# Kernel optimization log

Measured on AMD Instinct MI355X. Metric: run time of the kernel, lower is better.

The kernel has to match this reference:

```python
import jax, jax.numpy as jnp
import numpy as np

K_CONV = 4
NUM_HEADS = 16
NUM_KV_HEADS = 8
D_HEAD = 128
ROPE_THETA = 10000.0
EPS = 1e-6
NEG_INF = -1e30


def canon_b(x, w):
    """Canon-B: causal depthwise conv1d (kernel K_CONV) with residual.
    x: [B, S, C], w: [C, K_CONV]. out[t] = x[t] + sum_k w[:,k] * x[t-k]."""
    S = x.shape[1]
    xp = jnp.pad(x, ((0, 0), (K_CONV - 1, 0), (0, 0)))
    conv = sum(xp[:, K_CONV - 1 - k:K_CONV - 1 - k + S, :] * w[:, k] for k in range(K_CONV))
    return x + conv


def rms_norm(x, w):
    var = jnp.mean(x * x, axis=-1, keepdims=True)
    return x * jax.lax.rsqrt(var + EPS) * w


def rope_cos_sin(S, d):
    inv_freq = 1.0 / (ROPE_THETA ** (jnp.arange(0, d, 2, dtype=jnp.float32) / d))
    freqs = jnp.arange(S, dtype=jnp.float32)[:, None] * inv_freq  # [S, d/2]
    emb = jnp.concatenate([freqs, freqs], axis=-1)  # [S, d]
    return jnp.cos(emb), jnp.sin(emb)


def rotate_half(x):
    x1, x2 = jnp.split(x, 2, axis=-1)
    return jnp.concatenate([-x2, x1], axis=-1)


def setup_inputs() -> dict:
    key = jax.random.key(0)
    ks = jax.random.split(key, 8)
    B, S, D = 2, 2048, 2048
    Dkv = NUM_KV_HEADS * D_HEAD
    s = 0.02
    return {
        "hidden_states": jax.random.normal(ks[0], (B, S, D), jnp.float32),
        "Wq": jax.random.normal(ks[1], (D, D), jnp.float32) * s,
        "Wk": jax.random.normal(ks[2], (Dkv, D), jnp.float32) * s,
        "Wv": jax.random.normal(ks[3], (Dkv, D), jnp.float32) * s,
        "Wo": jax.random.normal(ks[4], (D, D), jnp.float32) * s,
        "canon_q_w": jax.random.normal(ks[5], (D, K_CONV), jnp.float32) * 0.1,
        "canon_k_w": jax.random.normal(ks[6], (Dkv, K_CONV), jnp.float32) * 0.1,
        "canon_v_w": jax.random.normal(ks[7], (Dkv, K_CONV), jnp.float32) * 0.1,
        "q_norm_w": jnp.ones((D_HEAD,), jnp.float32),
        "k_norm_w": jnp.ones((D_HEAD,), jnp.float32),
    }


def reference(hidden_states, Wq, Wk, Wv, Wo, canon_q_w, canon_k_w, canon_v_w, q_norm_w, k_norm_w):
    B, S, D = hidden_states.shape
    scale = 1.0 / np.sqrt(D_HEAD)
    groups = NUM_HEADS // NUM_KV_HEADS

    # QKV projections (no bias)
    q = hidden_states @ Wq.T
    k = hidden_states @ Wk.T
    v = hidden_states @ Wv.T

    # Canon-B causal depthwise conv on flat projections
    q = canon_b(q, canon_q_w)
    k = canon_b(k, canon_k_w)
    v = canon_b(v, canon_v_w)

    # Split heads: [B, S, H, d_head]
    q = q.reshape(B, S, NUM_HEADS, D_HEAD)
    k = k.reshape(B, S, NUM_KV_HEADS, D_HEAD)
    v = v.reshape(B, S, NUM_KV_HEADS, D_HEAD)

    # qk RMSNorm over d_head
    q = rms_norm(q, q_norm_w)
    k = rms_norm(k, k_norm_w)

    # RoPE
    cos, sin = rope_cos_sin(S, D_HEAD)  # [S, d_head]
    cos = cos[None, :, None, :]
    sin = sin[None, :, None, :]
    q = q * cos + rotate_half(q) * sin
    k = k * cos + rotate_half(k) * sin

    # [B, H, S, d_head]
    q = q.transpose(0, 2, 1, 3)
    k = k.transpose(0, 2, 1, 3)
    v = v.transpose(0, 2, 1, 3)

    # GQA: repeat kv heads
    k = jnp.repeat(k, groups, axis=1)
    v = jnp.repeat(v, groups, axis=1)

    # Causal attention (eager)
    scores = jnp.einsum("bhqd,bhkd->bhqk", q, k) * scale
    causal = jnp.tril(jnp.ones((S, S), bool))
    scores = jnp.where(causal, scores, NEG_INF)
    probs = jax.nn.softmax(scores, axis=-1)
    attn = jnp.einsum("bhqk,bhkd->bhqd", probs, v)

    out = attn.transpose(0, 2, 1, 3).reshape(B, S, D)
    return out @ Wo.T
```

## Files before the change

### kernel.cpp

```cpp
#include <hip/hip_runtime.h>
#include <hip/hip_bf16.h>

typedef __bf16 bf16;
typedef __bf16 bf16x8 __attribute__((ext_vector_type(8)));
typedef float  floatx4 __attribute__((ext_vector_type(4)));

#define AS1 __attribute__((address_space(1)))
#define AS3 __attribute__((address_space(3)))

#define B_    2
#define S_    2048
#define D_    2048
#define H_    16
#define KVH_  8
#define DH_   128
#define M_    4096
#define NQKV_ 4096

__global__ __launch_bounds__(256) void prep_kernel(const float* __restrict__ hidden,
                                                   const float* __restrict__ Wq,
                                                   const float* __restrict__ Wk,
                                                   const float* __restrict__ Wv,
                                                   const float* __restrict__ Wo,
                                                   bf16* __restrict__ X,
                                                   bf16* __restrict__ Wcat,
                                                   bf16* __restrict__ Wob,
                                                   float* __restrict__ cost,
                                                   float* __restrict__ sint) {
    size_t u = (size_t)blockIdx.x * 256 + threadIdx.x;
    if (u < 5242880) {
        const float* src; bf16* dst; size_t off;
        if (u < 2097152)      { src = hidden; dst = X;              off = u; }
        else if (u < 3145728) { src = Wq;     dst = Wcat;           off = u - 2097152; }
        else if (u < 3670016) { src = Wk;     dst = Wcat + 4194304; off = u - 3145728; }
        else if (u < 4194304) { src = Wv;     dst = Wcat + 6291456; off = u - 3670016; }
        else                  { src = Wo;     dst = Wob;            off = u - 4194304; }
        float4 v = *(const float4*)(src + off * 4);
        union { bf16 h[4]; double d; } uu;
        uu.h[0] = (bf16)v.x; uu.h[1] = (bf16)v.y; uu.h[2] = (bf16)v.z; uu.h[3] = (bf16)v.w;
        *(double*)(dst + off * 4) = uu.d;
    } else {
        int r = (int)(u - 5242880);
        int t = r >> 6, fi = r & 63;
        float inv = expf(-9.210340371976184f * (float)fi * (1.0f / 64.0f));
        float ang = (float)t * inv;
        cost[r] = cosf(ang);
        sint[r] = sinf(ang);
    }
}

__global__ __launch_bounds__(512, 2) void gemm_bt8(const bf16* __restrict__ A,
                                                   const bf16* __restrict__ Bw,
                                                   bf16* __restrict__ C,
                                                   int M, int N, int K) {
    __shared__ __align__(16) bf16 Als[4][256 * 32];
    __shared__ __align__(16) bf16 Bls[4][256 * 32];
    int tid  = threadIdx.x;
    int wave = tid >> 6, lane = tid & 63;
    int quad = lane >> 4, l16 = lane & 15;
    int wr = wave >> 2, wc = wave & 3;

    int nbx = N >> 8;
    int wg  = (blockIdx.x & 7) * ((int)gridDim.x >> 3) + (blockIdx.x >> 3);
    int by  = wg / nbx, bx = wg % nbx;
    long bm0 = (long)by << 8, bn0 = (long)bx << 8;

    int slot8 = ((quad ^ ((l16 ^ (l16 >> 2)) & 3)) << 3);

    int srow   = tid >> 2;
    int schunk = (tid & 3) ^ ((srow ^ (srow >> 2)) & 3);
    const bf16* Asrc = A  + (bm0 + srow) * K + schunk * 8;
    const bf16* Bsrc = Bw + (bn0 + srow) * K + schunk * 8;
    size_t ldoff = (size_t)128 * K;

    floatx4 acc[8][4] = {};
    int NT = K >> 5;

#define STAGE_A8(t) { int d_ = (t) & 3; long k0_ = (long)(t) << 5;                                   \
    __builtin_amdgcn_global_load_lds((AS1 const unsigned int*)(Asrc + k0_),                          \
                                     (AS3 unsigned int*)(&Als[d_][0] + tid * 8), 16, 0, 0);          \
    __builtin_amdgcn_global_load_lds((AS1 const unsigned int*)(Asrc + ldoff + k0_),                  \
                                     (AS3 unsigned int*)(&Als[d_][0] + tid * 8 + 4096), 16, 0, 0); }
#define STAGE_B8(t) { int d_ = (t) & 3; long k0_ = (long)(t) << 5;                                   \
    __builtin_amdgcn_global_load_lds((AS1 const unsigned int*)(Bsrc + k0_),                          \
                                     (AS3 unsigned int*)(&Bls[d_][0] + tid * 8), 16, 0, 0);          \
    __builtin_amdgcn_global_load_lds((AS1 const unsigned int*)(Bsrc + ldoff + k0_),                  \
                                     (AS3 unsigned int*)(&Bls[d_][0] + tid * 8 + 4096), 16, 0, 0); }

    STAGE_A8(0); STAGE_B8(0);
    STAGE_A8(1); STAGE_B8(1);
    STAGE_A8(2); STAGE_B8(2);
    asm volatile("s_waitcnt vmcnt(8)" ::: "memory");
    __builtin_amdgcn_s_barrier();

    for (int u = 0; u < NT; ++u) {
        const bf16* Ab = &Als[u & 3][0];
        const bf16* Bb = &Bls[u & 3][0];
        bf16x8 af[8], bfr[4];
        #pragma unroll
        for (int mt = 0; mt < 8; ++mt) {
            int row = wr * 128 + mt * 16 + l16;
            af[mt] = *(const bf16x8*)(Ab + row * 32 + slot8);
        }
        #pragma unroll
        for (int nt = 0; nt < 4; ++nt) {
            int col = wc * 64 + nt * 16 + l16;
            bfr[nt] = *(const bf16x8*)(Bb + col * 32 + slot8);
        }
        if (u + 3 < NT) { STAGE_A8(u + 3); STAGE_B8(u + 3); }
        #pragma unroll
        for (int mt = 0; mt < 8; ++mt)
            #pragma unroll
            for (int nt = 0; nt < 4; ++nt)
                acc[mt][nt] = __builtin_amdgcn_mfma_f32_16x16x32_bf16(af[mt], bfr[nt], acc[mt][nt], 0, 0, 0);
        if (u < NT - 3)       { asm volatile("s_waitcnt vmcnt(8)" ::: "memory"); }
        else if (u == NT - 3) { asm volatile("s_waitcnt vmcnt(4)" ::: "memory"); }
        else                  { asm volatile("s_waitcnt vmcnt(0)" ::: "memory"); }
        __builtin_amdgcn_s_barrier();
    }
#undef STAGE_A8
#undef STAGE_B8
    #pragma unroll
    for (int mt = 0; mt < 8; ++mt) {
        #pragma unroll
        for (int nt = 0; nt < 4; ++nt) {
            long row = bm0 + wr * 128 + mt * 16 + quad * 4;
            long col = bn0 + wc * 64 + nt * 16 + l16;
            #pragma unroll
            for (int r = 0; r < 4; ++r)
                C[(row + r) * N + col] = (bf16)acc[mt][nt][r];
        }
    }
}

#define BM 128
#define BN 128
#define BK 64
template <typename CT>
__global__ __launch_bounds__(256) void gemm_bt(const bf16* __restrict__ A,
                                               const bf16* __restrict__ Bw,
                                               CT* __restrict__ C,
                                               int M, int N, int K) {
    __shared__ __align__(16) bf16 Als[BM * BK];
    __shared__ __align__(16) bf16 Bls[BN * BK];
    int tid  = threadIdx.x;
    int wave = tid >> 6, lane = tid & 63;
    int quad = lane >> 4, l16 = lane & 15;
    int wm = (wave >> 1) << 6;
    int wn = (wave & 1) << 6;

    long bm0 = (long)blockIdx.y * BM;
    long bn0 = (long)blockIdx.x * BN;
    const bf16* Ab = A  + bm0 * K;
    const bf16* Bb = Bw + bn0 * K;

    int srow = wave * 32 + (lane >> 3);
    int scol = ((lane & 7) ^ (lane >> 3)) << 3;
    int sdst = (wave * 32 + (lane >> 3)) * BK + ((lane & 7) << 3);

    floatx4 acc[4][4] = {};

    for (int k0 = 0; k0 < K; k0 += BK) {
        #pragma unroll
        for (int i = 0; i < 4; ++i) {
            const bf16* ga = Ab + (long)(srow + i * 8) * K + k0 + scol;
            const bf16* gb = Bb + (long)(srow + i * 8) * K + k0 + scol;
            __builtin_amdgcn_global_load_lds((AS1 const unsigned int*)ga,
                                             (AS3 unsigned int*)(Als + sdst + i * 512), 16, 0, 0);
            __builtin_amdgcn_global_load_lds((AS1 const unsigned int*)gb,
                                             (AS3 unsigned int*)(Bls + sdst + i * 512), 16, 0, 0);
        }
        __syncthreads();
        #pragma unroll
        for (int ks = 0; ks < 2; ++ks) {
            bf16x8 af[4], bfr[4];
            #pragma unroll
            for (int t = 0; t < 4; ++t) {
                int row = wm + t * 16 + l16;
                int g = (ks * 4 + quad) ^ (row & 7);
                af[t] = *(const bf16x8*)(Als + row * BK + (g << 3));
            }
            #pragma unroll
            for (int t = 0; t < 4; ++t) {
                int row = wn + t * 16 + l16;
                int g = (ks * 4 + quad) ^ (row & 7);
                bfr[t] = *(const bf16x8*)(Bls + row * BK + (g << 3));
            }
            #pragma unroll
            for (int mt = 0; mt < 4; ++mt)
                #pragma unroll
                for (int nt = 0; nt < 4; ++nt)
                    acc[mt][nt] = __builtin_amdgcn_mfma_f32_16x16x32_bf16(af[mt], bfr[nt], acc[mt][nt], 0, 0, 0);
        }
        __syncthreads();
    }
    #pragma unroll
    for (int mt = 0; mt < 4; ++mt) {
        #pragma unroll
        for (int nt = 0; nt < 4; ++nt) {
            long row = bm0 + wm + mt * 16 + quad * 4;
            long col = bn0 + wn + nt * 16 + l16;
            #pragma unroll
            for (int r = 0; r < 4; ++r)
                C[(row + r) * N + col] = (CT)acc[mt][nt][r];
        }
    }
}

__global__ __launch_bounds__(256, 4) void canon_kernel(const bf16* __restrict__ QKV,
                                                       const float* __restrict__ wq,
                                                       const float* __restrict__ wk,
                                                       const float* __restrict__ wv,
                                                       const float* __restrict__ qnw,
                                                       const float* __restrict__ knw,
                                                       const float* __restrict__ cost,
                                                       const float* __restrict__ sint,
                                                       bf16* __restrict__ qf,
                                                       bf16* __restrict__ kf,
                                                       bf16* __restrict__ vfrag) {
    __shared__ __align__(16) bf16 vtile[32 * 520];
    int tid  = threadIdx.x;
    int wid  = blockIdx.x * 4 + (tid >> 6);
    int lane = tid & 63;
    int b  = wid >> 11;
    int g  = (wid >> 8) & 7;
    int c  = wid & 255;
    int t0 = c << 3;
    int ch = (g << 9) + (lane << 3);

    const float* wrow; int cw;
    if (g < 4)      { wrow = wq; cw = ch; }
    else if (g < 6) { wrow = wk; cw = ch - 2048; }
    else            { wrow = wv; cw = ch - 3072; }

    float4 w4[8];
    #pragma unroll
    for (int j = 0; j < 8; ++j) w4[j] = *(const float4*)(wrow + (cw + j) * 4);

    union U8 { float4 v; bf16 h[8]; };
    const bf16* srcb = QKV + (size_t)((b << 11) + t0) * 4096 + ch;

    float xm1[8], xm2[8], xm3[8];
    if (t0 > 0) {
        U8 u1, u2, u3;
        u1.v = *(const float4*)(srcb - 4096);
        u2.v = *(const float4*)(srcb - 2 * 4096);
        u3.v = *(const float4*)(srcb - 3 * 4096);
        #pragma unroll
        for (int i = 0; i < 8; ++i) {
            xm1[i] = (float)u1.h[i]; xm2[i] = (float)u2.h[i]; xm3[i] = (float)u3.h[i];
        }
    } else {
        #pragma unroll
        for (int i = 0; i < 8; ++i) { xm1[i] = 0.f; xm2[i] = 0.f; xm3[i] = 0.f; }
    }

    float4 nxtv = *(const float4*)(srcb);

    if (g < 6) {
        int j0   = ch & 127;
        int head = (g < 4) ? (ch >> 7) : ((ch - 2048) >> 7);
        const float* nw = (g < 4) ? qnw : knw;
        float nwv[8];
        {
            float4 na = *(const float4*)(nw + j0);
            float4 nb = *(const float4*)(nw + j0 + 4);
            #pragma unroll
            for (int i = 0; i < 8; ++i) nwv[i] = (i < 4) ? (&na.x)[i] : (&nb.x)[i - 4];
        }
        int ks = (lane >> 2) & 3, qd = lane & 3;
        size_t qkbase = ((size_t)((g < 4 ? (b << 4) : (b << 3)) + head) << 18)
                      + ((size_t)(t0 >> 4) << 11) + ((size_t)ks << 9)
                      + ((size_t)qd << 7) + ((size_t)(t0 & 15) << 3);
        bf16* dstb = (g < 4 ? qf : kf) + qkbase;

        int fi0 = j0 & 63;
        bool neg = (j0 < 64);
        const float* ctp = cost + t0 * 64 + fi0;
        const float* stp = sint + t0 * 64 + fi0;

        #pragma unroll
        for (int tt = 0; tt < 8; ++tt) {
            U8 u; u.v = nxtv;
            if (tt < 7) nxtv = *(const float4*)(srcb + (size_t)(tt + 1) * 4096);
            float cur[8], cv[8];
            #pragma unroll
            for (int i = 0; i < 8; ++i) cur[i] = (float)u.h[i];
            #pragma unroll
            for (int i = 0; i < 8; ++i) {
                float a = fmaf(w4[i].x, cur[i], cur[i]);
                a = fmaf(w4[i].y, xm1[i], a);
                a = fmaf(w4[i].z, xm2[i], a);
                cv[i] = fmaf(w4[i].w, xm3[i], a);
                xm3[i] = xm2[i]; xm2[i] = xm1[i]; xm1[i] = cur[i];
            }
            float ss = 0.f;
            #pragma unroll
            for (int i = 0; i < 8; ++i) ss = fmaf(cv[i], cv[i], ss);
            ss += __shfl_xor(ss, 1); ss += __shfl_xor(ss, 2);
            ss += __shfl_xor(ss, 4); ss += __shfl_xor(ss, 8);
            float r1 = rsqrtf(ss * (1.0f / 128.0f) + 1e-6f);
            float xn[8];
            #pragma unroll
            for (int i = 0; i < 8; ++i) xn[i] = cv[i] * r1 * nwv[i];
            float4 ca = *(const float4*)(ctp + tt * 64);
            float4 cb = *(const float4*)(ctp + tt * 64 + 4);
            float4 sa = *(const float4*)(stp + tt * 64);
            float4 sb = *(const float4*)(stp + tt * 64 + 4);
            __align__(16) bf16 outv[8];
            #pragma unroll
            for (int i = 0; i < 8; ++i) {
                float xp  = __shfl_xor(xn[i], 8);
                float rot = neg ? -xp : xp;
                float cc = (i < 4) ? (&ca.x)[i] : (&cb.x)[i - 4];
                float sn = (i < 4) ? (&sa.x)[i] : (&sb.x)[i - 4];
                outv[i] = (bf16)fmaf(xn[i], cc, rot * sn);
            }
            *(float4*)(dstb + (tt << 3)) = *(const float4*)outv;
        }
    } else {
        int lrow0 = (tid >> 6) << 3;
        #pragma unroll
        for (int tt = 0; tt < 8; ++tt) {
            U8 u; u.v = nxtv;
            if (tt < 7) nxtv = *(const float4*)(srcb + (size_t)(tt + 1) * 4096);
            float cur[8];
            __align__(16) bf16 outv[8];
            #pragma unroll
            for (int i = 0; i < 8; ++i) cur[i] = (float)u.h[i];
            #pragma unroll
            for (int i = 0; i < 8; ++i) {
                float a = fmaf(w4[i].x, cur[i], cur[i]);
                a = fmaf(w4[i].y, xm1[i], a);
                a = fmaf(w4[i].z, xm2[i], a);
                a = fmaf(w4[i].w, xm3[i], a);
                xm3[i] = xm2[i]; xm2[i] = xm1[i]; xm1[i] = cur[i];
                outv[i] = (bf16)a;
            }
            *(float4*)(&vtile[(lrow0 + tt) * 520 + (lane << 3)]) = *(const float4*)outv;
        }
        __syncthreads();
        int T  = (((blockIdx.x * 4) & 255) << 3);
        int kt = T >> 6, ks = (T >> 5) & 1;
        int hb = (g - 6) << 2;
        #pragma unroll
        for (int p = 0; p < 8; ++p) {
            int cidx = tid + p * 256;
            int hd  = cidx >> 9;
            int dnt = (cidx >> 6) & 7;
            int lc  = cidx & 63;
            int quad = lc >> 4, l16 = lc & 15;
            int scol = hd * 128 + dnt * 16 + l16;
            __align__(16) bf16 outv[8];
            #pragma unroll
            for (int j = 0; j < 8; ++j)
                outv[j] = vtile[(quad * 8 + j) * 520 + scol];
            size_t off = (((size_t)(b * 8 + hb + hd) * 32 + kt) << 13)
                       + ((size_t)ks << 12) + ((size_t)dnt << 9) + ((size_t)lc << 3);
            *(float4*)(vfrag + off) = *(const float4*)outv;
        }
    }
}

__global__ __launch_bounds__(256) void flash_attn(const bf16* __restrict__ qf,
                                                  const bf16* __restrict__ kf,
                                                  const bf16* __restrict__ vfrag,
                                                  bf16* __restrict__ attn) {
    __shared__ __align__(16) bf16 Kls[2][8192];
    __shared__ __align__(16) bf16 Vls[2][8192];
    __shared__ __align__(16) bf16 Pls[4][16][72];
    int lid  = blockIdx.x;
    int pair = lid & 15;
    int b    = pair >> 3, kvh = pair & 7;
    int inner = lid >> 4;
    int qt   = 31 - (inner >> 1);
    int h    = kvh * 2 + (inner & 1);
    int tid = threadIdx.x, wave = tid >> 6, lane = tid & 63;
    int quad = lane >> 4, l16 = lane & 15;
    int qrow0 = (qt << 6) + (wave << 4);

    const bf16* kfp = kf    + (((size_t)b * KVH_ + kvh) << 18);
    const bf16* vfp = vfrag + (((size_t)b * KVH_ + kvh) << 18);
    const bf16* qfp = qf    + ((((size_t)(b * H_ + h) * 128 + (qt << 2) + wave)) << 11);

    bf16x8 aq[4];
    #pragma unroll
    for (int ks = 0; ks < 4; ++ks)
        aq[ks] = *(const bf16x8*)(qfp + (ks << 9) + (lane << 3));

    floatx4 o[8] = {};
    float l_i[4] = {0.f, 0.f, 0.f, 0.f};
    const float scl2 = 0.08838834764831845f * 1.4426950408889634f;

    int ktiles = qt + 1;
    int eo = tid << 3;

    #pragma unroll
    for (int i = 0; i < 4; ++i) {
        __builtin_amdgcn_global_load_lds((AS1 const unsigned int*)(kfp + eo + (i << 11)),
                                         (AS3 unsigned int*)(&Kls[0][0] + eo + (i << 11)), 16, 0, 0);
        __builtin_amdgcn_global_load_lds((AS1 const unsigned int*)(vfp + eo + (i << 11)),
                                         (AS3 unsigned int*)(&Vls[0][0] + eo + (i << 11)), 16, 0, 0);
    }

    int cur = 0;
    for (int kt = 0; kt < ktiles; ++kt) {
        __syncthreads();
        if (kt + 1 < ktiles) {
            const bf16* ksrc = kfp + (((size_t)(kt + 1)) << 13) + eo;
            const bf16* vsrc = vfp + (((size_t)(kt + 1)) << 13) + eo;
            bf16* kd = &Kls[cur ^ 1][0] + eo;
            bf16* vd = &Vls[cur ^ 1][0] + eo;
            #pragma unroll
            for (int i = 0; i < 4; ++i) {
                __builtin_amdgcn_global_load_lds((AS1 const unsigned int*)(ksrc + (i << 11)),
                                                 (AS3 unsigned int*)(kd + (i << 11)), 16, 0, 0);
                __builtin_amdgcn_global_load_lds((AS1 const unsigned int*)(vsrc + (i << 11)),
                                                 (AS3 unsigned int*)(vd + (i << 11)), 16, 0, 0);
            }
        }
        const bf16* Kb = &Kls[cur][0];
        const bf16* Vb = &Vls[cur][0];
        floatx4 sc[4] = {};
        #pragma unroll
        for (int nt = 0; nt < 4; ++nt) {
            #pragma unroll
            for (int ks = 0; ks < 4; ++ks) {
                bf16x8 kb8 = *(const bf16x8*)(Kb + ((nt * 4 + ks) << 9) + (lane << 3));
                sc[nt] = __builtin_amdgcn_mfma_f32_16x16x32_bf16(aq[ks], kb8, sc[nt], 0, 0, 0);
            }
        }
        int qr0 = qrow0 + (quad << 2);
        int kb = kt << 6;
        if (kt == ktiles - 1) {
            #pragma unroll
            for (int nt = 0; nt < 4; ++nt) {
                int key = kb + nt * 16 + l16;
                #pragma unroll
                for (int r = 0; r < 4; ++r) {
                    float pv = exp2f(sc[nt][r] * scl2);
                    pv = (key <= qr0 + r) ? pv : 0.f;
                    l_i[r] += pv;
                    Pls[wave][(quad << 2) + r][nt * 16 + l16] = (bf16)pv;
                }
            }
        } else {
            #pragma unroll
            for (int nt = 0; nt < 4; ++nt) {
                #pragma unroll
                for (int r = 0; r < 4; ++r) {
                    float pv = exp2f(sc[nt][r] * scl2);
                    l_i[r] += pv;
                    Pls[wave][(quad << 2) + r][nt * 16 + l16] = (bf16)pv;
                }
            }
        }
        {
            bf16x8 pa = *(const bf16x8*)(&Pls[wave][l16][(quad << 3)]);
            #pragma unroll
            for (int dnt = 0; dnt < 8; ++dnt) {
                bf16x8 vb = *(const bf16x8*)(Vb + ((size_t)dnt << 9) + (lane << 3));
                o[dnt] = __builtin_amdgcn_mfma_f32_16x16x32_bf16(pa, vb, o[dnt], 0, 0, 0);
            }
            bf16x8 pb = *(const bf16x8*)(&Pls[wave][l16][32 + (quad << 3)]);
            #pragma unroll
            for (int dnt = 0; dnt < 8; ++dnt) {
                bf16x8 vb = *(const bf16x8*)(Vb + ((size_t)(8 + dnt) << 9) + (lane << 3));
                o[dnt] = __builtin_amdgcn_mfma_f32_16x16x32_bf16(pb, vb, o[dnt], 0, 0, 0);
            }
        }
        cur ^= 1;
    }
    #pragma unroll
    for (int r = 0; r < 4; ++r) {
        float l = l_i[r];
        l += __shfl_xor(l, 1); l += __shfl_xor(l, 2);
        l += __shfl_xor(l, 4); l += __shfl_xor(l, 8);
        l_i[r] = 1.0f / l;
    }
    #pragma unroll
    for (int dnt = 0; dnt < 8; ++dnt) {
        #pragma unroll
        for (int r = 0; r < 4; ++r) {
            size_t row = (size_t)b * S_ + qrow0 + (quad << 2) + r;
            attn[row * D_ + h * DH_ + dnt * 16 + l16] = (bf16)(o[dnt][r] * l_i[r]);
        }
    }
}

extern "C" void kernel_launch(void* const* d_in, const int* in_sizes, int n_in,
                              void* d_out, int out_size, void* d_ws, size_t ws_size,
                              hipStream_t stream) {
    const float* hidden = (const float*)d_in[0];
    const float* Wq  = (const float*)d_in[1];
    const float* Wk  = (const float*)d_in[2];
    const float* Wv  = (const float*)d_in[3];
    const float* Wo  = (const float*)d_in[4];
    const float* cqw = (const float*)d_in[5];
    const float* ckw = (const float*)d_in[6];
    const float* cvw = (const float*)d_in[7];
    const float* qnw = (const float*)d_in[8];
    const float* knw = (const float*)d_in[9];

    char* p = (char*)d_ws;
    auto alloc = [&](size_t bytes) { char* r = p; p += (bytes + 255) & ~(size_t)255; return r; };
    bf16*  X    = (bf16*)alloc((size_t)M_ * D_ * 2);
    bf16*  Wcat = (bf16*)alloc((size_t)NQKV_ * D_ * 2);
    bf16*  Wob  = (bf16*)alloc((size_t)D_ * D_ * 2);
    bf16*  QKV  = (bf16*)alloc((size_t)M_ * NQKV_ * 2);
    bf16*  qfb  = (bf16*)alloc((size_t)B_ * H_ * S_ * DH_ * 2);
    bf16*  kfb  = (bf16*)alloc((size_t)B_ * KVH_ * S_ * DH_ * 2);
    bf16*  vfr  = (bf16*)alloc((size_t)B_ * KVH_ * S_ * DH_ * 2);
    float* cost = (float*)alloc((size_t)S_ * 64 * 4);
    float* sint = (float*)alloc((size_t)S_ * 64 * 4);
    bf16*  attnb = QKV;

    prep_kernel<<<20992, 256, 0, stream>>>(hidden, Wq, Wk, Wv, Wo, X, Wcat, Wob, cost, sint);
    gemm_bt8<<<(M_ / 256) * (NQKV_ / 256), 512, 0, stream>>>(X, Wcat, QKV, M_, NQKV_, D_);
    canon_kernel<<<1024, 256, 0, stream>>>(QKV, cqw, ckw, cvw, qnw, knw, cost, sint, qfb, kfb, vfr);
    flash_attn<<<1024, 256, 0, stream>>>(qfb, kfb, vfr, attnb);
    gemm_bt<float><<<dim3(D_ / BN, M_ / BM), 256, 0, stream>>>(attnb, Wob, (float*)d_out, M_, D_, D_);
}
```

Before: 338.6 us.

## Replace output projection GEMM with 4-stage pipelined 256x128 tile kernel

The Wo projection GEMM moves from a simple 128x128 tile kernel with a single LDS buffer and two barriers per K step to a 512-thread kernel with 256x128 tiles. It uses a 4-deep LDS ring filled by async global-to-LDS loads and a single barrier per iteration, with XOR-swizzled LDS layout and a grouped block-index remap for L2 locality. The aim is to hide global-memory latency behind MFMA work and raise per-block reuse. The cost is only 256 blocks for M=4096, N=2048, which may underfill the GPU, plus higher register pressure.

Result: no change. 345.0 us (+1.9%).

```diff
diff --git a/kernel.cpp b/kernel.cpp
--- a/kernel.cpp
+++ b/kernel.cpp
@@ -133,76 +133,84 @@
     }
 }
 
-#define BM 128
-#define BN 128
-#define BK 64
-template <typename CT>
-__global__ __launch_bounds__(256) void gemm_bt(const bf16* __restrict__ A,
-                                               const bf16* __restrict__ Bw,
-                                               CT* __restrict__ C,
-                                               int M, int N, int K) {
-    __shared__ __align__(16) bf16 Als[BM * BK];
-    __shared__ __align__(16) bf16 Bls[BN * BK];
+__global__ __launch_bounds__(512, 2) void gemm_bt8f(const bf16* __restrict__ A,
+                                                    const bf16* __restrict__ Bw,
+                                                    float* __restrict__ C,
+                                                    int M, int N, int K) {
+    __shared__ __align__(16) bf16 Als[4][256 * 32];
+    __shared__ __align__(16) bf16 Bls[4][128 * 32];
     int tid  = threadIdx.x;
     int wave = tid >> 6, lane = tid & 63;
     int quad = lane >> 4, l16 = lane & 15;
-    int wm = (wave >> 1) << 6;
-    int wn = (wave & 1) << 6;
-
-    long bm0 = (long)blockIdx.y * BM;
-    long bn0 = (long)blockIdx.x * BN;
-    const bf16* Ab = A  + bm0 * K;
-    const bf16* Bb = Bw + bn0 * K;
-
-    int srow = wave * 32 + (lane >> 3);
-    int scol = ((lane & 7) ^ (lane >> 3)) << 3;
-    int sdst = (wave * 32 + (lane >> 3)) * BK + ((lane & 7) << 3);
-
-    floatx4 acc[4][4] = {};
-
-    for (int k0 = 0; k0 < K; k0 += BK) {
-        #pragma unroll
-        for (int i = 0; i < 4; ++i) {
-            const bf16* ga = Ab + (long)(srow + i * 8) * K + k0 + scol;
-            const bf16* gb = Bb + (long)(srow + i * 8) * K + k0 + scol;
-            __builtin_amdgcn_global_load_lds((AS1 const unsigned int*)ga,
-                                             (AS3 unsigned int*)(Als + sdst + i * 512), 16, 0, 0);
-            __builtin_amdgcn_global_load_lds((AS1 const unsigned int*)gb,
-                                             (AS3 unsigned int*)(Bls + sdst + i * 512), 16, 0, 0);
-        }
-        __syncthreads();
-        #pragma unroll
-        for (int ks = 0; ks < 2; ++ks) {
-            bf16x8 af[4], bfr[4];
-            #pragma unroll
-            for (int t = 0; t < 4; ++t) {
-                int row = wm + t * 16 + l16;
-                int g = (ks * 4 + quad) ^ (row & 7);
-                af[t] = *(const bf16x8*)(Als + row * BK + (g << 3));
-            }
-            #pragma unroll
-            for (int t = 0; t < 4; ++t) {
-                int row = wn + t * 16 + l16;
-                int g = (ks * 4 + quad) ^ (row & 7);
-                bfr[t] = *(const bf16x8*)(Bls + row * BK + (g << 3));
-            }
-            #pragma unroll
-            for (int mt = 0; mt < 4; ++mt)
-                #pragma unroll
-                for (int nt = 0; nt < 4; ++nt)
-                    acc[mt][nt] = __builtin_amdgcn_mfma_f32_16x16x32_bf16(af[mt], bfr[nt], acc[mt][nt], 0, 0, 0);
-        }
-        __syncthreads();
-    }
-    #pragma unroll
-    for (int mt = 0; mt < 4; ++mt) {
-        #pragma unroll
-        for (int nt = 0; nt < 4; ++nt) {
-            long row = bm0 + wm + mt * 16 + quad * 4;
-            long col = bn0 + wn + nt * 16 + l16;
+    int wr = wave >> 2, wc = wave & 3;
+
+    int nbx = N >> 7;
+    int wg  = (blockIdx.x & 7) * ((int)gridDim.x >> 3) + (blockIdx.x >> 3);
+    int by  = wg / nbx, bx = wg % nbx;
+    long bm0 = (long)by << 8, bn0 = (long)bx << 7;
+
+    int slot8 = ((quad ^ ((l16 ^ (l16 >> 2)) & 3)) << 3);
+
+    int srow   = tid >> 2;
+    int schunk = (tid & 3) ^ ((srow ^ (srow >> 2)) & 3);
+    const bf16* Asrc = A  + (bm0 + srow) * K + schunk * 8;
+    const bf16* Bsrc = Bw + (bn0 + srow) * K + schunk * 8;
+    size_t ldoff = (size_t)128 * K;
+
+    floatx4 acc[8][2] = {};
+    int NT = K >> 5;
+
+#define STAGE_AF(t) { int d_ = (t) & 3; long k0_ = (long)(t) << 5;                                   \
+    __builtin_amdgcn_global_load_lds((AS1 const unsigned int*)(Asrc + k0_),                          \
+                                     (AS3 unsigned int*)(&Als[d_][0] + tid * 8), 16, 0, 0);          \
+    __builtin_amdgcn_global_load_lds((AS1 const unsigned int*)(Asrc + ldoff + k0_),                  \
+                                     (AS3 unsigned int*)(&Als[d_][0] + tid * 8 + 4096), 16, 0, 0); }
+#define STAGE_BF(t) { int d_ = (t) & 3; long k0_ = (long)(t) << 5;                                   \
+    __builtin_amdgcn_global_load_lds((AS1 const unsigned int*)(Bsrc + k0_),                          \
+                                     (AS3 unsigned int*)(&Bls[d_][0] + tid * 8), 16, 0, 0); }
+
+    STAGE_AF(0); STAGE_BF(0);
+    STAGE_AF(1); STAGE_BF(1);
+    STAGE_AF(2); STAGE_BF(2);
+    asm volatile("s_waitcnt vmcnt(6)" ::: "memory");
+    __builtin_amdgcn_s_barrier();
+
+    for (int u = 0; u < NT; ++u) {
+        const bf16* Ab = &Als[u & 3][0];
+        const bf16* Bb = &Bls[u & 3][0];
+        bf16x8 af[8], bfr[2];
+        #pragma unroll
+        for (int mt = 0; mt < 8; ++mt) {
+            int row = wr * 128 + mt * 16 + l16;
+            af[mt] = *(const bf16x8*)(Ab + row * 32 + slot8);
+        }
+        #pragma unroll
+        for (int nt = 0; nt < 2; ++nt) {
+            int col = wc * 32 + nt * 16 + l16;
+            bfr[nt] = *(const bf16x8*)(Bb + col * 32 + slot8);
+        }
+        if (u + 3 < NT) { STAGE_AF(u + 3); STAGE_BF(u + 3); }
+        #pragma unroll
+        for (int mt = 0; mt < 8; ++mt)
+            #pragma unroll
+            for (int nt = 0; nt < 2; ++nt)
+                acc[mt][nt] = __builtin_amdgcn_mfma_f32_16x16x32_bf16(af[mt], bfr[nt], acc[mt][nt], 0, 0, 0);
+        if (u < NT - 3)       { asm volatile("s_waitcnt vmcnt(6)" ::: "memory"); }
+        else if (u == NT - 3) { asm volatile("s_waitcnt vmcnt(3)" ::: "memory"); }
+        else                  { asm volatile("s_waitcnt vmcnt(0)" ::: "memory"); }
+        __builtin_amdgcn_s_barrier();
+    }
+#undef STAGE_AF
+#undef STAGE_BF
+    #pragma unroll
+    for (int mt = 0; mt < 8; ++mt) {
+        #pragma unroll
+        for (int nt = 0; nt < 2; ++nt) {
+            long row = bm0 + wr * 128 + mt * 16 + quad * 4;
+            long col = bn0 + wc * 32 + nt * 16 + l16;
             #pragma unroll
             for (int r = 0; r < 4; ++r)
-                C[(row + r) * N + col] = (CT)acc[mt][nt][r];
+                C[(row + r) * N + col] = acc[mt][nt][r];
         }
     }
 }
@@ -519,5 +527,5 @@
     gemm_bt8<<<(M_ / 256) * (NQKV_ / 256), 512, 0, stream>>>(X, Wcat, QKV, M_, NQKV_, D_);
     canon_kernel<<<1024, 256, 0, stream>>>(QKV, cqw, ckw, cvw, qnw, knw, cost, sint, qfb, kfb, vfr);
     flash_attn<<<1024, 256, 0, stream>>>(qfb, kfb, vfr, attnb);
-    gemm_bt<float><<<dim3(D_ / BN, M_ / BM), 256, 0, stream>>>(attnb, Wob, (float*)d_out, M_, D_, D_);
+    gemm_bt8f<<<(M_ / 256) * (D_ / 128), 512, 0, stream>>>(attnb, Wob, (float*)d_out, M_, D_, D_);
 }
```
